# Optimization experiments

Hardware: AMD Instinct MI355X
Metric: run time of the kernel (lower is better)

## Reference

```python
import jax, jax.numpy as jnp
import numpy as np

N_NODES = 100_000
N_EDGES = 1_600_000
N_GRAPHS = 512
D_NODE = 128
H = 128
L_EXTRA = 2  # model_layer - 1


def _bn(x, g, b, eps=1e-5):
    # BatchNorm1d, training-mode math (biased batch variance), eval dropout = identity
    mu = jnp.mean(x, axis=0)
    var = jnp.var(x, axis=0)
    return g * (x - mu) * jax.lax.rsqrt(var + eps) + b


def _gin_conv(x, src, dst, W1, b1, bng, bnb, W2, b2):
    # GINConv (eps=0): mlp(x + sum_{j->i} x_j); mlp = Lin -> BN -> ReLU -> Lin
    agg = jax.ops.segment_sum(x[src], dst, num_segments=x.shape[0])
    h = x + agg
    h = jax.nn.relu(_bn(h @ W1 + b1, bng, bnb))
    return h @ W2 + b2


def setup_inputs():
    key = jax.random.key(0)
    ks = jax.random.split(key, 24)
    s = 0.05
    d = {}
    d["x"] = jax.random.normal(ks[0], (N_NODES, D_NODE), dtype=jnp.float32)
    d["edge_index"] = jax.random.randint(ks[1], (2, N_EDGES), 0, N_NODES, dtype=jnp.int32)
    d["batch"] = jnp.sort(jax.random.randint(ks[2], (N_NODES,), 0, N_GRAPHS, dtype=jnp.int32))
    d["vn_emb"] = jax.random.normal(ks[3], (1, H)) * s
    # conv1 MLP: Linear(D_NODE, 2H) -> BN -> ReLU -> Linear(2H, H)
    d["c1_W1"] = jax.random.normal(ks[4], (D_NODE, 2 * H)) * s
    d["c1_b1"] = jnp.zeros((2 * H,))
    d["c1_bng"] = jnp.ones((2 * H,))
    d["c1_bnb"] = jnp.zeros((2 * H,))
    d["c1_W2"] = jax.random.normal(ks[5], (2 * H, H)) * s
    d["c1_b2"] = jnp.zeros((H,))
    d["bn1_g"] = jnp.ones((H,))
    d["bn1_b"] = jnp.zeros((H,))
    # stacked extra GIN layers (model_layer - 1)
    d["cW1"] = jax.random.normal(ks[6], (L_EXTRA, H, 2 * H)) * s
    d["cb1"] = jnp.zeros((L_EXTRA, 2 * H))
    d["cbng"] = jnp.ones((L_EXTRA, 2 * H))
    d["cbnb"] = jnp.zeros((L_EXTRA, 2 * H))
    d["cW2"] = jax.random.normal(ks[7], (L_EXTRA, 2 * H, H)) * s
    d["cb2"] = jnp.zeros((L_EXTRA, H))
    d["bns_g"] = jnp.ones((L_EXTRA, H))
    d["bns_b"] = jnp.zeros((L_EXTRA, H))
    # virtual node MLP: Lin(H,2H)->BN->ReLU->Lin(2H,H)->BN->ReLU->Dropout
    d["vW1"] = jax.random.normal(ks[8], (H, 2 * H)) * s
    d["vb1"] = jnp.zeros((2 * H,))
    d["vbn1_g"] = jnp.ones((2 * H,))
    d["vbn1_b"] = jnp.zeros((2 * H,))
    d["vW2"] = jax.random.normal(ks[9], (2 * H, H)) * s
    d["vb2"] = jnp.zeros((H,))
    d["vbn2_g"] = jnp.ones((H,))
    d["vbn2_b"] = jnp.zeros((H,))
    return d


def reference(x, edge_index, batch, vn_emb, c1_W1, c1_b1, c1_bng, c1_bnb, c1_W2, c1_b2,
              bn1_g, bn1_b, cW1, cb1, cbng, cbnb, cW2, cb2, bns_g, bns_b,
              vW1, vb1, vbn1_g, vbn1_b, vW2, vb2, vbn2_g, vbn2_b):
    src, dst = edge_index[0], edge_index[1]
    # virtual node feature per graph: Embedding(1, H) indexed with zeros
    vfeat = jnp.broadcast_to(vn_emb[0], (N_GRAPHS, H))
    # layer 1: dropout is identity in eval mode
    post = jax.nn.relu(_bn(_gin_conv(x, src, dst, c1_W1, c1_b1, c1_bng, c1_bnb, c1_W2, c1_b2), bn1_g, bn1_b))
    for i in range(L_EXTRA):
        post = post + vfeat[batch]                       # virtual-node broadcast
        post = _bn(_gin_conv(post, src, dst, cW1[i], cb1[i], cbng[i], cbnb[i], cW2[i], cb2[i]), bns_g[i], bns_b[i])
        if i < L_EXTRA - 1:
            post = jax.nn.relu(post)
            pooled = jax.ops.segment_sum(post, batch, num_segments=N_GRAPHS)  # GlobalAddPool
            z = pooled + vfeat
            z = jax.nn.relu(_bn(z @ vW1 + vb1, vbn1_g, vbn1_b))
            vfeat = jax.nn.relu(_bn(z @ vW2 + vb2, vbn2_g, vbn2_b))
    # readout: global mean pool over nodes per graph
    counts = jax.ops.segment_sum(jnp.ones((x.shape[0],), post.dtype), batch, num_segments=N_GRAPHS)
    out = jax.ops.segment_sum(post, batch, num_segments=N_GRAPHS) / jnp.maximum(counts, 1.0)[:, None]
    return out
```

## Files before the change

### kernel.cpp

```cpp
#include <hip/hip_runtime.h>

#define NN 100000
#define NE 1600000
#define NG 512
#define DH 128
#define DH2 256
#define SCB 98
#define NSTRIPE 32

typedef __attribute__((ext_vector_type(8))) _Float16 h8;
typedef __attribute__((ext_vector_type(2))) _Float16 h2;
typedef __attribute__((ext_vector_type(4))) float f4;

static inline size_t align256(size_t x) { return (x + 255) & ~size_t(255); }

__global__ __launch_bounds__(256) void countslot_k(const int* __restrict__ ei,
                                                   int* __restrict__ cursor,
                                                   int* __restrict__ slot) {
    int i = blockIdx.x * blockDim.x + threadIdx.x;
    int stride = gridDim.x * blockDim.x;
    for (int e = i; e < NE; e += stride)
        slot[e] = atomicAdd(&cursor[ei[NE + e]], 1);
}

__global__ __launch_bounds__(256) void place_k(const int* __restrict__ ei,
                                               const int* __restrict__ rowptr,
                                               const int* __restrict__ slot,
                                               int* __restrict__ esrc) {
    int i = blockIdx.x * blockDim.x + threadIdx.x;
    int stride = gridDim.x * blockDim.x;
    for (int e = i; e < NE; e += stride)
        esrc[rowptr[ei[NE + e]] + slot[e]] = ei[e];
}

__global__ __launch_bounds__(256) void scan1_k(const int* __restrict__ deg,
                                               int* __restrict__ part) {
    int i0 = blockIdx.x * 1024 + threadIdx.x * 4;
    int s = 0;
    if (i0 < NN) {
        int4 v = *(const int4*)(deg + i0);
        s = v.x + v.y + v.z + v.w;
    }
#pragma unroll
    for (int o = 1; o < 64; o <<= 1) s += __shfl_xor(s, o);
    __shared__ int ws[4];
    if ((threadIdx.x & 63) == 0) ws[threadIdx.x >> 6] = s;
    __syncthreads();
    if (threadIdx.x == 0) part[blockIdx.x] = ws[0] + ws[1] + ws[2] + ws[3];
}

__global__ void scan2_k(int* __restrict__ part, int* __restrict__ rowptr,
                        const int* __restrict__ batch, int* __restrict__ gcnt) {
    int t = threadIdx.x;
    __shared__ int wtot[2];
    int v = 0, s = 0;
    if (t < 128) {
        v = (t < SCB) ? part[t] : 0;
        s = v;
#pragma unroll
        for (int o = 1; o < 64; o <<= 1) {
            int u = __shfl_up(s, o);
            if ((t & 63) >= o) s += u;
        }
        if ((t & 63) == 63) wtot[t >> 6] = s;
    }
    __syncthreads();
    if (t < 128) {
        if (t >= 64) s += wtot[0];
        if (t < SCB) part[t] = s - v;
        if (t == SCB - 1) rowptr[NN] = s;
    }
    for (int g = t; g < NG; g += 256) {
        int lo = 0, hi = NN;
        while (lo < hi) { int m = (lo + hi) >> 1; if (batch[m] < g) lo = m + 1; else hi = m; }
        int b0 = lo;
        lo = 0; hi = NN;
        int g1 = g + 1;
        while (lo < hi) { int m = (lo + hi) >> 1; if (batch[m] < g1) lo = m + 1; else hi = m; }
        gcnt[g] = lo - b0;
    }
}

__global__ __launch_bounds__(256) void scan3_k(const int* __restrict__ deg,
                                               const int* __restrict__ part,
                                               int* __restrict__ rowptr) {
    int t = threadIdx.x;
    int i0 = blockIdx.x * 1024 + t * 4;
    int4 v = {0, 0, 0, 0};
    if (i0 < NN) v = *(const int4*)(deg + i0);
    int s = v.x + v.y + v.z + v.w;
    __shared__ int sc[256];
    sc[t] = s;
    __syncthreads();
    for (int o = 1; o < 256; o <<= 1) {
        int add = (t >= o) ? sc[t - o] : 0;
        __syncthreads();
        sc[t] += add;
        __syncthreads();
    }
    int excl = (t ? sc[t - 1] : 0) + part[blockIdx.x];
    if (i0 < NN) {
        int4 r;
        r.x = excl;
        r.y = excl + v.x;
        r.z = excl + v.x + v.y;
        r.w = excl + v.x + v.y + v.z;
        *(int4*)(rowptr + i0) = r;
    }
}

__global__ void castx_k(const float* __restrict__ x, _Float16* __restrict__ xh,
                        const float* __restrict__ emb, _Float16* __restrict__ vfeat) {
    int i = blockIdx.x * blockDim.x + threadIdx.x;
    if (i < NG * 16) {
        const float* e = emb + (i & 15) * 8;
        h8 v = {(_Float16)e[0], (_Float16)e[1], (_Float16)e[2], (_Float16)e[3],
                (_Float16)e[4], (_Float16)e[5], (_Float16)e[6], (_Float16)e[7]};
        ((h8*)vfeat)[i] = v;
    }
    if (i >= NN * 16) return;
    const float4* s = (const float4*)x + i * 2;
    float4 p = s[0], q = s[1];
    h8 h = {(_Float16)p.x, (_Float16)p.y, (_Float16)p.z, (_Float16)p.w,
            (_Float16)q.x, (_Float16)q.y, (_Float16)q.z, (_Float16)q.w};
    ((h8*)xh)[i] = h;
}

__global__ void zin_k(const float* __restrict__ pooled, const _Float16* __restrict__ vf,
                      _Float16* __restrict__ zb) {
    int i = blockIdx.x * blockDim.x + threadIdx.x;
    if (i < NG * DH) zb[i] = (_Float16)(pooled[i] + (float)vf[i]);
}

__global__ void addvn_k(_Float16* __restrict__ x, const _Float16* __restrict__ vfeat,
                        const int* __restrict__ batch) {
    int i = blockIdx.x * blockDim.x + threadIdx.x;
    if (i >= NN * 16) return;
    int row = i >> 4;
    int bg = batch[row];
    h8 u = ((h8*)x)[i];
    h8 v = ((const h8*)vfeat)[bg * 16 + (i & 15)];
    h8 o;
#pragma unroll
    for (int e = 0; e < 8; e++) o[e] = (_Float16)((float)u[e] + (float)v[e]);
    ((h8*)x)[i] = o;
}

__global__ void finalout_k(const float* __restrict__ pooled2, const int* __restrict__ gcnt,
                           float* __restrict__ outp) {
    int i = blockIdx.x * blockDim.x + threadIdx.x;
    if (i >= NG * DH) return;
    float cnt = (float)gcnt[i >> 7];
    outp[i] = pooled2[i] / fmaxf(cnt, 1.0f);
}

struct WPack {
    const float* w[8];
    _Float16* wt[8];
    int K[8];
    int N[8];
};
__global__ void wtrans_k(WPack p) {
    int id = blockIdx.z;
    const float* W = p.w[id];
    _Float16* Wt = p.wt[id];
    int K = p.K[id], N = p.N[id];
    int n0 = blockIdx.x * 32, k0 = blockIdx.y * 32;
    if (n0 >= N || k0 >= K) return;
    __shared__ float t[32][33];
    int tx = threadIdx.x & 31, ty = threadIdx.x >> 5;
    for (int i = 0; i < 32; i += 8)
        t[ty + i][tx] = W[(size_t)(k0 + ty + i) * N + n0 + tx];
    __syncthreads();
    for (int i = 0; i < 32; i += 8)
        Wt[(size_t)(n0 + ty + i) * K + k0 + tx] = (_Float16)t[tx][ty + i];
}

__global__ __launch_bounds__(256) void agg_k(const _Float16* __restrict__ xin,
                                             const int* __restrict__ rowptr,
                                             const int* __restrict__ esrc,
                                             _Float16* __restrict__ out) {
    int wave = threadIdx.x >> 6, lane = threadIdx.x & 63;
    int node = blockIdx.x * 4 + wave;
    if (node >= NN) return;
    const h2* xr = (const h2*)xin;
    h2 self = xr[(size_t)node * 64 + lane];
    float a0 = (float)self.x, a1 = (float)self.y;
    int beg = rowptr[node], end = rowptr[node + 1];
    int j = beg;
    for (; j + 7 < end; j += 8) {
        int s0 = esrc[j],     s1 = esrc[j + 1], s2 = esrc[j + 2], s3 = esrc[j + 3];
        int s4 = esrc[j + 4], s5 = esrc[j + 5], s6 = esrc[j + 6], s7 = esrc[j + 7];
        h2 u0 = xr[(size_t)s0 * 64 + lane];
        h2 u1 = xr[(size_t)s1 * 64 + lane];
        h2 u2 = xr[(size_t)s2 * 64 + lane];
        h2 u3 = xr[(size_t)s3 * 64 + lane];
        h2 u4 = xr[(size_t)s4 * 64 + lane];
        h2 u5 = xr[(size_t)s5 * 64 + lane];
        h2 u6 = xr[(size_t)s6 * 64 + lane];
        h2 u7 = xr[(size_t)s7 * 64 + lane];
        a0 += ((float)u0.x + (float)u1.x) + ((float)u2.x + (float)u3.x)
            + ((float)u4.x + (float)u5.x) + ((float)u6.x + (float)u7.x);
        a1 += ((float)u0.y + (float)u1.y) + ((float)u2.y + (float)u3.y)
            + ((float)u4.y + (float)u5.y) + ((float)u6.y + (float)u7.y);
    }
    for (; j < end; j++) {
        h2 u = xr[(size_t)esrc[j] * 64 + lane];
        a0 += (float)u.x; a1 += (float)u.y;
    }
    h2 o; o.x = (_Float16)a0; o.y = (_Float16)a1;
    ((h2*)out)[(size_t)node * 64 + lane] = o;
}

__global__ __launch_bounds__(256, 3) void gemmA_k(
        const _Float16* __restrict__ A, const _Float16* __restrict__ Wt,
        const float* __restrict__ bias, _Float16* __restrict__ C,
        float* __restrict__ csum, float* __restrict__ csq, int M) {
    constexpr int K = 128, NCF = 256;
    constexpr int LDA = K + 8;
    __shared__ __align__(16) _Float16 As[64 * LDA];
    __shared__ __align__(16) _Float16 Ws[128 * LDA];
    const int tid = threadIdx.x;
    const int lane = tid & 63;
    const int wave = tid >> 6;
    const int wr = wave >> 1;
    const int wc = wave & 1;
    const int lm = lane & 15, lq = lane >> 4;
    const int mB = blockIdx.x * 64;

    const int sr = tid >> 4;
    const int sc = (tid & 15) * 8;
#pragma unroll
    for (int rr = 0; rr < 64; rr += 16) {
        int gr = mB + rr + sr; if (gr >= M) gr = M - 1;
        *(h8*)&As[(rr + sr) * LDA + sc] = *(const h8*)&A[(size_t)gr * K + sc];
    }
#pragma unroll
    for (int rr = 0; rr < 128; rr += 16)
        *(h8*)&Ws[(rr + sr) * LDA + sc] = *(const h8*)&Wt[(size_t)(rr + sr) * K + sc];
    __syncthreads();

    f4 acc[2][8];
#pragma unroll
    for (int i = 0; i < 2; i++)
#pragma unroll
        for (int jj = 0; jj < 8; jj++) acc[i][jj] = (f4){0.f, 0.f, 0.f, 0.f};
#pragma unroll
    for (int ct = 0; ct < 2; ct++) {
        if (ct) {
            __syncthreads();
#pragma unroll
            for (int rr = 0; rr < 128; rr += 16)
                *(h8*)&Ws[(rr + sr) * LDA + sc] =
                    *(const h8*)&Wt[(size_t)(128 + rr + sr) * K + sc];
            __syncthreads();
        }
#pragma unroll
        for (int ks = 0; ks < 4; ks++) {
            h8 af[2], bf[4];
#pragma unroll
            for (int i = 0; i < 2; i++)
                af[i] = *(const h8*)&As[(wr * 32 + i * 16 + lm) * LDA + ks * 32 + lq * 8];
#pragma unroll
            for (int j = 0; j < 4; j++)
                bf[j] = *(const h8*)&Ws[(wc * 64 + j * 16 + lm) * LDA + ks * 32 + lq * 8];
#pragma unroll
            for (int i = 0; i < 2; i++)
#pragma unroll
                for (int j = 0; j < 4; j++)
                    acc[i][ct * 4 + j] =
                        __builtin_amdgcn_mfma_f32_16x16x32_f16(af[i], bf[j], acc[i][ct * 4 + j], 0, 0, 0);
        }
    }

    float bv[8];
#pragma unroll
    for (int jj = 0; jj < 8; jj++) bv[jj] = bias[(jj >> 2) * 128 + wc * 64 + (jj & 3) * 16 + lm];
    float ls[8] = {0, 0, 0, 0, 0, 0, 0, 0}, lsq[8] = {0, 0, 0, 0, 0, 0, 0, 0};
    _Float16* Cs = As;
    const int trow = tid >> 4;
    const int tcol = (tid & 15) * 8;
#pragma unroll
    for (int half = 0; half < 2; half++) {
        __syncthreads();
#pragma unroll
        for (int i = 0; i < 2; i++) {
            int row = wr * 32 + i * 16 + lq * 4;
#pragma unroll
            for (int j = 0; j < 4; j++) {
                int jj = half * 4 + j;
#pragma unroll
                for (int r = 0; r < 4; r++) {
                    float v = acc[i][jj][r] + bv[jj];
                    Cs[(row + r) * LDA + wc * 64 + j * 16 + lm] = (_Float16)v;
                    if (mB + row + r < M) { ls[jj] += v; lsq[jj] += v * v; }
                }
            }
        }
        __syncthreads();
#pragma unroll
        for (int p = 0; p < 4; p++) {
            int row = p * 16 + trow;
            int grow = mB + row;
            if (grow < M) {
                h8 v = *(const h8*)&Cs[row * LDA + tcol];
                *(h8*)&C[(size_t)grow * NCF + half * 128 + tcol] = v;
            }
        }
    }
    const int stripe = blockIdx.x & (NSTRIPE - 1);
#pragma unroll
    for (int jj = 0; jj < 8; jj++) {
        float s = ls[jj], q = lsq[jj];
        s += __shfl_xor(s, 16); s += __shfl_xor(s, 32);
        q += __shfl_xor(q, 16); q += __shfl_xor(q, 32);
        if (lq == 0) {
            int col = (jj >> 2) * 128 + wc * 64 + (jj & 3) * 16 + lm;
            atomicAdd(&csum[stripe * NCF + col], s);
            atomicAdd(&csq[stripe * NCF + col], q);
        }
    }
}

__global__ __launch_bounds__(256, 3) void gemmB_k(
        const _Float16* __restrict__ A, const _Float16* __restrict__ Wt,
        const float* __restrict__ bias, _Float16* __restrict__ C,
        float* __restrict__ csum, float* __restrict__ csq, int M,
        const float* __restrict__ csumIn, const float* __restrict__ csqIn,
        const float* __restrict__ g, const float* __restrict__ b) {
    constexpr int K = 256, NCF = 128, BK = 128;
    constexpr int LDA = BK + 8;
    constexpr int LDW = BK + 4;
    __shared__ __align__(16) _Float16 As[64 * LDA];
    __shared__ __align__(16) _Float16 Ws[128 * LDW];
    __shared__ float s_sc[256], s_sh[256];
    const int tid = threadIdx.x;
    const int lane = tid & 63;
    const int wave = tid >> 6;
    const int wr = wave >> 1;
    const int wc = wave & 1;
    const int lm = lane & 15, lq = lane >> 4;
    const int mB = blockIdx.x * 64;
    const int n0 = wc * 64;

    {
        float s = 0.f, q = 0.f;
        for (int st = 0; st < NSTRIPE; st++) {
            s += csumIn[st * 256 + tid];
            q += csqIn[st * 256 + tid];
        }
        float invM = 1.0f / (float)M;
        float mean = s * invM;
        float var = q * invM - mean * mean;
        float scv = g[tid] * rsqrtf(var + 1e-5f);
        s_sc[tid] = scv;
        s_sh[tid] = b[tid] - mean * scv;
    }
    __syncthreads();

    f4 acc[2][4];
#pragma unroll
    for (int i = 0; i < 2; i++)
#pragma unroll
        for (int j = 0; j < 4; j++) acc[i][j] = (f4){0.f, 0.f, 0.f, 0.f};

    const int sr = tid >> 4;
    const int sc = (tid & 15) * 8;

    for (int kc = 0; kc < K; kc += BK) {
        if (kc) __syncthreads();
        float bscv[8], bshv[8];
#pragma unroll
        for (int e = 0; e < 8; e++) {
            bscv[e] = s_sc[kc + sc + e];
            bshv[e] = s_sh[kc + sc + e];
        }
#pragma unroll
        for (int rr = 0; rr < 64; rr += 16) {
            int gr = mB + rr + sr; if (gr >= M) gr = M - 1;
            h8 h = *(const h8*)&A[(size_t)gr * K + kc + sc];
#pragma unroll
            for (int e = 0; e < 8; e++)
                h[e] = (_Float16)fmaxf((float)h[e] * bscv[e] + bshv[e], 0.f);
            *(h8*)&As[(rr + sr) * LDA + sc] = h;
        }
#pragma unroll
        for (int rr = 0; rr < 128; rr += 16)
            *(h8*)&Ws[(rr + sr) * LDW + sc] =
                *(const h8*)&Wt[(size_t)(rr + sr) * K + kc + sc];
        __syncthreads();
#pragma unroll
        for (int ks = 0; ks < BK / 32; ks++) {
            h8 af[2], bf[4];
#pragma unroll
            for (int i = 0; i < 2; i++)
                af[i] = *(const h8*)&As[(wr * 32 + i * 16 + lm) * LDA + ks * 32 + lq * 8];
#pragma unroll
            for (int j = 0; j < 4; j++)
                bf[j] = *(const h8*)&Ws[(n0 + j * 16 + lm) * LDW + ks * 32 + lq * 8];
#pragma unroll
            for (int i = 0; i < 2; i++)
#pragma unroll
                for (int j = 0; j < 4; j++)
                    acc[i][j] = __builtin_amdgcn_mfma_f32_16x16x32_f16(af[i], bf[j], acc[i][j], 0, 0, 0);
        }
    }

    float bv[4];
#pragma unroll
    for (int j = 0; j < 4; j++) bv[j] = bias[n0 + j * 16 + lm];
    float ls[4] = {0, 0, 0, 0}, lsq[4] = {0, 0, 0, 0};
    __syncthreads();
    _Float16* Cs = As;
#pragma unroll
    for (int i = 0; i < 2; i++) {
        int row = wr * 32 + i * 16 + lq * 4;
        bool rv[4];
#pragma unroll
        for (int r = 0; r < 4; r++) rv[r] = (mB + row + r) < M;
#pragma unroll
        for (int j = 0; j < 4; j++) {
#pragma unroll
            for (int r = 0; r < 4; r++) {
                float v = acc[i][j][r] + bv[j];
                Cs[(row + r) * LDA + wc * 64 + j * 16 + lm] = (_Float16)v;
                if (rv[r]) { ls[j] += v; lsq[j] += v * v; }
            }
        }
    }
    const int stripe = blockIdx.x & (NSTRIPE - 1);
#pragma unroll
    for (int j = 0; j < 4; j++) {
        float s = ls[j], q = lsq[j];
        s += __shfl_xor(s, 16); s += __shfl_xor(s, 32);
        q += __shfl_xor(q, 16); q += __shfl_xor(q, 32);
        if (lq == 0) {
            atomicAdd(&csum[stripe * NCF + n0 + j * 16 + lm], s);
            atomicAdd(&csq[stripe * NCF + n0 + j * 16 + lm], q);
        }
    }
    __syncthreads();
    const int trow = tid >> 4;
    const int tcol = (tid & 15) * 8;
#pragma unroll
    for (int p = 0; p < 4; p++) {
        int row = p * 16 + trow;
        int grow = mB + row;
        if (grow < M) {
            h8 v = *(const h8*)&Cs[row * LDA + tcol];
            *(h8*)&C[(size_t)grow * NCF + tcol] = v;
        }
    }
}

__global__ void bnrelu_k(const _Float16* __restrict__ in, _Float16* __restrict__ out,
                         const float* __restrict__ csum, const float* __restrict__ csq,
                         const float* __restrict__ g, const float* __restrict__ b,
                         const _Float16* __restrict__ vfeat, const int* __restrict__ batch,
                         int M) {
    constexpr int PER = 16;
    __shared__ float s_sc[128], s_sh[128];
    if (threadIdx.x < 128) {
        int col = threadIdx.x;
        float s = 0.f, q = 0.f;
        for (int st = 0; st < NSTRIPE; st++) {
            s += csum[st * 128 + col];
            q += csq[st * 128 + col];
        }
        float invM = 1.0f / (float)M;
        float mean = s * invM;
        float var = q * invM - mean * mean;
        float scv = g[col] * rsqrtf(var + 1e-5f);
        s_sc[col] = scv;
        s_sh[col] = b[col] - mean * scv;
    }
    __syncthreads();
    int tid = blockIdx.x * blockDim.x + threadIdx.x;
    int c8 = tid % PER;
    int c0 = c8 * 8;
    float sc[8], sh[8];
#pragma unroll
    for (int e = 0; e < 8; e++) { sc[e] = s_sc[c0 + e]; sh[e] = s_sh[c0 + e]; }
    int total = M * PER;
    int stride = gridDim.x * blockDim.x;
    for (int i = tid; i < total; i += stride) {
        int row = i / PER;
        h8 u = ((const h8*)in)[i];
        h8 w;
        bool vn = (vfeat != nullptr);
        if (vn) w = ((const h8*)vfeat)[batch[row] * PER + c8];
        h8 o;
#pragma unroll
        for (int e = 0; e < 8; e++) {
            float vv = fmaxf((float)u[e] * sc[e] + sh[e], 0.f);
            if (vn) vv += (float)w[e];
            o[e] = (_Float16)vv;
        }
        ((h8*)out)[i] = o;
    }
}

__global__ __launch_bounds__(256) void bnpool_k(
        const _Float16* __restrict__ in, _Float16* __restrict__ out,
        const float* __restrict__ csum, const float* __restrict__ csq,
        const float* __restrict__ g, const float* __restrict__ b,
        const int* __restrict__ batch, float* __restrict__ pooled,
        int M, int relu) {
    __shared__ float s_sc[128], s_sh[128];
    if (threadIdx.x < 128) {
        int col = threadIdx.x;
        float s = 0.f, q = 0.f;
        for (int st = 0; st < NSTRIPE; st++) {
            s += csum[st * 128 + col];
            q += csq[st * 128 + col];
        }
        float invM = 1.0f / (float)M;
        float mean = s * invM;
        float var = q * invM - mean * mean;
        float scv = g[col] * rsqrtf(var + 1e-5f);
        s_sc[col] = scv;
        s_sh[col] = b[col] - mean * scv;
    }
    __syncthreads();
    int t = threadIdx.x;
    int c0 = (t & 63) * 2;
    int r0 = blockIdx.x * 128 + (t >> 6) * 32;
    float sc0 = s_sc[c0], h0 = s_sh[c0];
    float sc1 = s_sc[c0 + 1], h1 = s_sh[c0 + 1];
    int rend = r0 + 32; if (rend > M) rend = M;
    float a0 = 0.f, a1 = 0.f; int cur = -1;
    int r = r0;
    for (; r + 1 < rend; r += 2) {
        h2 ua = ((const h2*)in)[(size_t)r * 64 + (c0 >> 1)];
        h2 ub = ((const h2*)in)[(size_t)(r + 1) * 64 + (c0 >> 1)];
        int bga = batch[r], bgb = batch[r + 1];
        float va0 = (float)ua.x * sc0 + h0, va1 = (float)ua.y * sc1 + h1;
        float vb0 = (float)ub.x * sc0 + h0, vb1 = (float)ub.y * sc1 + h1;
        if (relu) {
            va0 = fmaxf(va0, 0.f); va1 = fmaxf(va1, 0.f);
            vb0 = fmaxf(vb0, 0.f); vb1 = fmaxf(vb1, 0.f);
        }
        if (out) {
            h2 oa; oa.x = (_Float16)va0; oa.y = (_Float16)va1;
            h2 ob; ob.x = (_Float16)vb0; ob.y = (_Float16)vb1;
            ((h2*)out)[(size_t)r * 64 + (c0 >> 1)] = oa;
            ((h2*)out)[(size_t)(r + 1) * 64 + (c0 >> 1)] = ob;
        }
        if (bga != cur) {
            if (cur >= 0) {
                atomicAdd(&pooled[(size_t)cur * DH + c0], a0);
                atomicAdd(&pooled[(size_t)cur * DH + c0 + 1], a1);
            }
            cur = bga; a0 = 0.f; a1 = 0.f;
        }
        a0 += va0; a1 += va1;
        if (bgb != cur) {
            atomicAdd(&pooled[(size_t)cur * DH + c0], a0);
            atomicAdd(&pooled[(size_t)cur * DH + c0 + 1], a1);
            cur = bgb; a0 = 0.f; a1 = 0.f;
        }
        a0 += vb0; a1 += vb1;
    }
    for (; r < rend; r++) {
        h2 u = ((const h2*)in)[(size_t)r * 64 + (c0 >> 1)];
        float v0 = (float)u.x * sc0 + h0;
        float v1 = (float)u.y * sc1 + h1;
        if (relu) { v0 = fmaxf(v0, 0.f); v1 = fmaxf(v1, 0.f); }
        if (out) { h2 o; o.x = (_Float16)v0; o.y = (_Float16)v1; ((h2*)out)[(size_t)r * 64 + (c0 >> 1)] = o; }
        int bg = batch[r];
        if (bg != cur) {
            if (cur >= 0) {
                atomicAdd(&pooled[(size_t)cur * DH + c0], a0);
                atomicAdd(&pooled[(size_t)cur * DH + c0 + 1], a1);
            }
            cur = bg; a0 = 0.f; a1 = 0.f;
        }
        a0 += v0; a1 += v1;
    }
    if (cur >= 0) {
        atomicAdd(&pooled[(size_t)cur * DH + c0], a0);
        atomicAdd(&pooled[(size_t)cur * DH + c0 + 1], a1);
    }
}

extern "C" void kernel_launch(void* const* d_in, const int* in_sizes, int n_in,
                              void* d_out, int out_size, void* d_ws, size_t ws_size,
                              hipStream_t stream) {
    const float* x      = (const float*)d_in[0];
    const int*   ei     = (const int*)d_in[1];
    const int*   batch  = (const int*)d_in[2];
    const float* vn_emb = (const float*)d_in[3];
    const float* c1_W1  = (const float*)d_in[4];
    const float* c1_b1  = (const float*)d_in[5];
    const float* c1_bng = (const float*)d_in[6];
    const float* c1_bnb = (const float*)d_in[7];
    const float* c1_W2  = (const float*)d_in[8];
    const float* c1_b2  = (const float*)d_in[9];
    const float* bn1_g  = (const float*)d_in[10];
    const float* bn1_b  = (const float*)d_in[11];
    const float* cW1    = (const float*)d_in[12];
    const float* cb1    = (const float*)d_in[13];
    const float* cbng   = (const float*)d_in[14];
    const float* cbnb   = (const float*)d_in[15];
    const float* cW2    = (const float*)d_in[16];
    const float* cb2    = (const float*)d_in[17];
    const float* bns_g  = (const float*)d_in[18];
    const float* bns_b  = (const float*)d_in[19];
    const float* vW1    = (const float*)d_in[20];
    const float* vb1    = (const float*)d_in[21];
    const float* vbn1_g = (const float*)d_in[22];
    const float* vbn1_b = (const float*)d_in[23];
    const float* vW2    = (const float*)d_in[24];
    const float* vb2    = (const float*)d_in[25];
    const float* vbn2_g = (const float*)d_in[26];
    const float* vbn2_b = (const float*)d_in[27];
    float* outp = (float*)d_out;
    (void)in_sizes; (void)n_in; (void)out_size; (void)ws_size;

    char* w = (char*)d_ws;
    size_t off = 0;
    auto carve = [&](size_t bytes) -> void* {
        void* p = w + off; off = align256(off + bytes); return p;
    };
    int*   cursor  = (int*)carve((size_t)NN * 4);
    float* pooled  = (float*)carve((size_t)NG * DH * 4);
    float* pooled2 = (float*)carve((size_t)NG * DH * 4);
    float *sA[3], *qA[3], *sB[3], *qB[3], *sV1, *qV1, *sV2, *qV2;
    for (int i = 0; i < 3; i++) {
        sA[i] = (float*)carve((size_t)NSTRIPE * 256 * 4);
        qA[i] = (float*)carve((size_t)NSTRIPE * 256 * 4);
    }
    for (int i = 0; i < 3; i++) {
        sB[i] = (float*)carve((size_t)NSTRIPE * 128 * 4);
        qB[i] = (float*)carve((size_t)NSTRIPE * 128 * 4);
    }
    sV1 = (float*)carve((size_t)NSTRIPE * 256 * 4);
    qV1 = (float*)carve((size_t)NSTRIPE * 256 * 4);
    sV2 = (float*)carve((size_t)NSTRIPE * 128 * 4);
    qV2 = (float*)carve((size_t)NSTRIPE * 128 * 4);
    size_t zbytes = off;
    int*   gcnt    = (int*)carve((size_t)NG * 4);
    int*   rowptr  = (int*)carve((size_t)(NN + 1) * 4);
    int*   slot    = (int*)carve((size_t)NE * 4);
    int*   esrc    = (int*)carve((size_t)NE * 4);
    int*   part    = (int*)carve((size_t)SCB * 4);
    _Float16* vfeat = (_Float16*)carve((size_t)NG * DH * 2);
    _Float16* zin   = (_Float16*)carve((size_t)NG * DH * 2);
    _Float16* zb    = (_Float16*)carve((size_t)NG * DH2 * 2);
    _Float16* vraw  = (_Float16*)carve((size_t)NG * DH * 2);
    _Float16* xh    = (_Float16*)carve((size_t)NN * DH * 2);
    _Float16* hb    = (_Float16*)carve((size_t)NN * DH * 2);
    _Float16* b1    = (_Float16*)carve((size_t)NN * DH2 * 2);
    _Float16* abuf  = (_Float16*)carve((size_t)NN * DH * 2);
    _Float16* Wt[8];
    for (int i = 0; i < 8; i++) Wt[i] = (_Float16*)carve((size_t)DH * DH2 * 2);

    WPack wp;
    wp.w[0] = c1_W1;            wp.K[0] = 128; wp.N[0] = 256;
    wp.w[1] = c1_W2;            wp.K[1] = 256; wp.N[1] = 128;
    wp.w[2] = cW1;              wp.K[2] = 128; wp.N[2] = 256;
    wp.w[3] = cW2;              wp.K[3] = 256; wp.N[3] = 128;
    wp.w[4] = cW1 + 128 * 256;  wp.K[4] = 128; wp.N[4] = 256;
    wp.w[5] = cW2 + 256 * 128;  wp.K[5] = 256; wp.N[5] = 128;
    wp.w[6] = vW1;              wp.K[6] = 128; wp.N[6] = 256;
    wp.w[7] = vW2;              wp.K[7] = 256; wp.N[7] = 128;
    for (int i = 0; i < 8; i++) wp.wt[i] = Wt[i];

    const int GB64 = (NN + 63) / 64;
    const int GB   = (NN + 127) / 128;
    const int GV64 = (NG + 63) / 64;

    hipMemsetAsync(d_ws, 0, zbytes, stream);
    countslot_k<<<782, 256, 0, stream>>>(ei, cursor, slot);
    scan1_k<<<SCB, 256, 0, stream>>>(cursor, part);
    scan2_k<<<1, 256, 0, stream>>>(part, rowptr, batch, gcnt);
    scan3_k<<<SCB, 256, 0, stream>>>(cursor, part, rowptr);
    place_k<<<782, 256, 0, stream>>>(ei, rowptr, slot, esrc);
    wtrans_k<<<dim3(8, 8, 8), 256, 0, stream>>>(wp);
    castx_k<<<(NN * 16 + 255) / 256, 256, 0, stream>>>(x, xh, vn_emb, vfeat);

    agg_k<<<NN / 4, 256, 0, stream>>>(xh, rowptr, esrc, hb);
    gemmA_k<<<GB64, 256, 0, stream>>>(hb, Wt[0], c1_b1, b1, sA[0], qA[0], NN);
    gemmB_k<<<GB64, 256, 0, stream>>>(b1, Wt[1], c1_b2, abuf, sB[0], qB[0], NN,
                                      sA[0], qA[0], c1_bng, c1_bnb);
    bnrelu_k<<<2048, 256, 0, stream>>>(abuf, abuf, sB[0], qB[0], bn1_g, bn1_b,
                                       vfeat, batch, NN);

    agg_k<<<NN / 4, 256, 0, stream>>>(abuf, rowptr, esrc, hb);
    gemmA_k<<<GB64, 256, 0, stream>>>(hb, Wt[2], cb1, b1, sA[1], qA[1], NN);
    gemmB_k<<<GB64, 256, 0, stream>>>(b1, Wt[3], cb2, abuf, sB[1], qB[1], NN,
                                      sA[1], qA[1], cbng, cbnb);
    bnpool_k<<<GB, 256, 0, stream>>>(abuf, abuf, sB[1], qB[1], bns_g, bns_b,
                                     batch, pooled, NN, 1);

    zin_k<<<(NG * DH + 255) / 256, 256, 0, stream>>>(pooled, vfeat, zin);
    gemmA_k<<<GV64, 256, 0, stream>>>(zin, Wt[6], vb1, zb, sV1, qV1, NG);
    gemmB_k<<<GV64, 256, 0, stream>>>(zb, Wt[7], vb2, vraw, sV2, qV2, NG,
                                      sV1, qV1, vbn1_g, vbn1_b);
    bnrelu_k<<<32, 256, 0, stream>>>(vraw, vfeat, sV2, qV2, vbn2_g, vbn2_b,
                                     nullptr, nullptr, NG);

    addvn_k<<<(NN * 16 + 255) / 256, 256, 0, stream>>>(abuf, vfeat, batch);
    agg_k<<<NN / 4, 256, 0, stream>>>(abuf, rowptr, esrc, hb);
    gemmA_k<<<GB64, 256, 0, stream>>>(hb, Wt[4], cb1 + 256, b1, sA[2], qA[2], NN);
    gemmB_k<<<GB64, 256, 0, stream>>>(b1, Wt[5], cb2 + 128, abuf, sB[2], qB[2], NN,
                                      sA[2], qA[2], cbng + 256, cbnb + 256);
    bnpool_k<<<GB, 256, 0, stream>>>(abuf, nullptr, sB[2], qB[2],
                                     bns_g + 128, bns_b + 128, batch, pooled2, NN, 0);

    finalout_k<<<(NG * DH + 255) / 256, 256, 0, stream>>>(pooled2, gcnt, outp);
}
```

Before: 703.8 us.

## Recompute first GEMM instead of storing the 256-wide intermediate to global memory

The first MLP GEMM now runs twice. A stats-only pass accumulates the BatchNorm sums without writing the intermediate. A fused kernel then recomputes it, applies BN and ReLU in shared memory, and runs the second GEMM straight from there. This removes the write and re-read of the NN×256 fp16 intermediate buffer. The cost is doubled first-GEMM compute, more shared memory, and lower occupancy (launch bounds drop from 3 to 2 blocks per CU).

```diff
diff --git a/kernel.cpp b/kernel.cpp
--- a/kernel.cpp
+++ b/kernel.cpp
@@ -212,11 +212,11 @@
     ((h2*)out)[(size_t)node * 64 + lane] = o;
 }
 
-__global__ __launch_bounds__(256, 3) void gemmA_k(
+__global__ __launch_bounds__(256, 3) void gemmS_k(
         const _Float16* __restrict__ A, const _Float16* __restrict__ Wt,
-        const float* __restrict__ bias, _Float16* __restrict__ C,
+        const float* __restrict__ bias,
         float* __restrict__ csum, float* __restrict__ csq, int M) {
-    constexpr int K = 128, NCF = 256;
+    constexpr int K = 128;
     constexpr int LDA = K + 8;
     __shared__ __align__(16) _Float16 As[64 * LDA];
     __shared__ __align__(16) _Float16 Ws[128 * LDA];
@@ -277,34 +277,17 @@
 #pragma unroll
     for (int jj = 0; jj < 8; jj++) bv[jj] = bias[(jj >> 2) * 128 + wc * 64 + (jj & 3) * 16 + lm];
     float ls[8] = {0, 0, 0, 0, 0, 0, 0, 0}, lsq[8] = {0, 0, 0, 0, 0, 0, 0, 0};
-    _Float16* Cs = As;
-    const int trow = tid >> 4;
-    const int tcol = (tid & 15) * 8;
-#pragma unroll
-    for (int half = 0; half < 2; half++) {
-        __syncthreads();
-#pragma unroll
-        for (int i = 0; i < 2; i++) {
-            int row = wr * 32 + i * 16 + lq * 4;
-#pragma unroll
-            for (int j = 0; j < 4; j++) {
-                int jj = half * 4 + j;
-#pragma unroll
-                for (int r = 0; r < 4; r++) {
+#pragma unroll
+    for (int i = 0; i < 2; i++) {
+        int row = wr * 32 + i * 16 + lq * 4;
+#pragma unroll
+        for (int jj = 0; jj < 8; jj++) {
+#pragma unroll
+            for (int r = 0; r < 4; r++) {
+                if (mB + row + r < M) {
                     float v = acc[i][jj][r] + bv[jj];
-                    Cs[(row + r) * LDA + wc * 64 + j * 16 + lm] = (_Float16)v;
-                    if (mB + row + r < M) { ls[jj] += v; lsq[jj] += v * v; }
+                    ls[jj] += v; lsq[jj] += v * v;
                 }
-            }
-        }
-        __syncthreads();
-#pragma unroll
-        for (int p = 0; p < 4; p++) {
-            int row = p * 16 + trow;
-            int grow = mB + row;
-            if (grow < M) {
-                h8 v = *(const h8*)&Cs[row * LDA + tcol];
-                *(h8*)&C[(size_t)grow * NCF + half * 128 + tcol] = v;
             }
         }
     }
@@ -316,23 +299,25 @@
         q += __shfl_xor(q, 16); q += __shfl_xor(q, 32);
         if (lq == 0) {
             int col = (jj >> 2) * 128 + wc * 64 + (jj & 3) * 16 + lm;
-            atomicAdd(&csum[stripe * NCF + col], s);
-            atomicAdd(&csq[stripe * NCF + col], q);
-        }
-    }
-}
-
-__global__ __launch_bounds__(256, 3) void gemmB_k(
-        const _Float16* __restrict__ A, const _Float16* __restrict__ Wt,
-        const float* __restrict__ bias, _Float16* __restrict__ C,
+            atomicAdd(&csum[stripe * 256 + col], s);
+            atomicAdd(&csq[stripe * 256 + col], q);
+        }
+    }
+}
+
+__global__ __launch_bounds__(256, 2) void gemmF_k(
+        const _Float16* __restrict__ A,
+        const _Float16* __restrict__ Wt1,
+        const _Float16* __restrict__ Wt2,
+        const float* __restrict__ b1v,
+        const float* __restrict__ b2v,
+        _Float16* __restrict__ C,
         float* __restrict__ csum, float* __restrict__ csq, int M,
         const float* __restrict__ csumIn, const float* __restrict__ csqIn,
         const float* __restrict__ g, const float* __restrict__ b) {
-    constexpr int K = 256, NCF = 128, BK = 128;
-    constexpr int LDA = BK + 8;
-    constexpr int LDW = BK + 4;
-    __shared__ __align__(16) _Float16 As[64 * LDA];
-    __shared__ __align__(16) _Float16 Ws[128 * LDW];
+    constexpr int LDA = 136, LDH = 264;
+    __shared__ __align__(16) _Float16 Hx[64 * LDH];
+    __shared__ __align__(16) _Float16 Ws[128 * LDA];
     __shared__ float s_sc[256], s_sh[256];
     const int tid = threadIdx.x;
     const int lane = tid & 63;
@@ -341,7 +326,6 @@
     const int wc = wave & 1;
     const int lm = lane & 15, lq = lane >> 4;
     const int mB = blockIdx.x * 64;
-    const int n0 = wc * 64;
 
     {
         float s = 0.f, q = 0.f;
@@ -356,62 +340,118 @@
         s_sc[tid] = scv;
         s_sh[tid] = b[tid] - mean * scv;
     }
-    __syncthreads();
-
-    f4 acc[2][4];
-#pragma unroll
-    for (int i = 0; i < 2; i++)
-#pragma unroll
-        for (int j = 0; j < 4; j++) acc[i][j] = (f4){0.f, 0.f, 0.f, 0.f};
 
     const int sr = tid >> 4;
     const int sc = (tid & 15) * 8;
-
-    for (int kc = 0; kc < K; kc += BK) {
-        if (kc) __syncthreads();
-        float bscv[8], bshv[8];
-#pragma unroll
-        for (int e = 0; e < 8; e++) {
-            bscv[e] = s_sc[kc + sc + e];
-            bshv[e] = s_sh[kc + sc + e];
-        }
-#pragma unroll
-        for (int rr = 0; rr < 64; rr += 16) {
-            int gr = mB + rr + sr; if (gr >= M) gr = M - 1;
-            h8 h = *(const h8*)&A[(size_t)gr * K + kc + sc];
-#pragma unroll
-            for (int e = 0; e < 8; e++)
-                h[e] = (_Float16)fmaxf((float)h[e] * bscv[e] + bshv[e], 0.f);
-            *(h8*)&As[(rr + sr) * LDA + sc] = h;
-        }
-#pragma unroll
-        for (int rr = 0; rr < 128; rr += 16)
-            *(h8*)&Ws[(rr + sr) * LDW + sc] =
-                *(const h8*)&Wt[(size_t)(rr + sr) * K + kc + sc];
-        __syncthreads();
-#pragma unroll
-        for (int ks = 0; ks < BK / 32; ks++) {
+#pragma unroll
+    for (int rr = 0; rr < 64; rr += 16) {
+        int gr = mB + rr + sr; if (gr >= M) gr = M - 1;
+        *(h8*)&Hx[(rr + sr) * LDA + sc] = *(const h8*)&A[(size_t)gr * 128 + sc];
+    }
+#pragma unroll
+    for (int rr = 0; rr < 128; rr += 16)
+        *(h8*)&Ws[(rr + sr) * LDA + sc] = *(const h8*)&Wt1[(size_t)(rr + sr) * 128 + sc];
+    __syncthreads();
+
+    f4 acc[2][8];
+#pragma unroll
+    for (int i = 0; i < 2; i++)
+#pragma unroll
+        for (int jj = 0; jj < 8; jj++) acc[i][jj] = (f4){0.f, 0.f, 0.f, 0.f};
+#pragma unroll
+    for (int ct = 0; ct < 2; ct++) {
+        if (ct) {
+            __syncthreads();
+#pragma unroll
+            for (int rr = 0; rr < 128; rr += 16)
+                *(h8*)&Ws[(rr + sr) * LDA + sc] =
+                    *(const h8*)&Wt1[(size_t)(128 + rr + sr) * 128 + sc];
+            __syncthreads();
+        }
+#pragma unroll
+        for (int ks = 0; ks < 4; ks++) {
             h8 af[2], bf[4];
 #pragma unroll
             for (int i = 0; i < 2; i++)
-                af[i] = *(const h8*)&As[(wr * 32 + i * 16 + lm) * LDA + ks * 32 + lq * 8];
+                af[i] = *(const h8*)&Hx[(wr * 32 + i * 16 + lm) * LDA + ks * 32 + lq * 8];
 #pragma unroll
             for (int j = 0; j < 4; j++)
-                bf[j] = *(const h8*)&Ws[(n0 + j * 16 + lm) * LDW + ks * 32 + lq * 8];
+                bf[j] = *(const h8*)&Ws[(wc * 64 + j * 16 + lm) * LDA + ks * 32 + lq * 8];
 #pragma unroll
             for (int i = 0; i < 2; i++)
 #pragma unroll
                 for (int j = 0; j < 4; j++)
-                    acc[i][j] = __builtin_amdgcn_mfma_f32_16x16x32_f16(af[i], bf[j], acc[i][j], 0, 0, 0);
-        }
-    }
-
-    float bv[4];
-#pragma unroll
-    for (int j = 0; j < 4; j++) bv[j] = bias[n0 + j * 16 + lm];
+                    acc[i][ct * 4 + j] =
+                        __builtin_amdgcn_mfma_f32_16x16x32_f16(af[i], bf[j], acc[i][ct * 4 + j], 0, 0, 0);
+        }
+    }
+    __syncthreads();
+
+    {
+        float bv1[8];
+#pragma unroll
+        for (int jj = 0; jj < 8; jj++)
+            bv1[jj] = b1v[(jj >> 2) * 128 + wc * 64 + (jj & 3) * 16 + lm];
+#pragma unroll
+        for (int i = 0; i < 2; i++) {
+            int row = wr * 32 + i * 16 + lq * 4;
+#pragma unroll
+            for (int jj = 0; jj < 8; jj++) {
+                int col = (jj >> 2) * 128 + wc * 64 + (jj & 3) * 16 + lm;
+                float scv = s_sc[col], shv = s_sh[col];
+#pragma unroll
+                for (int r = 0; r < 4; r++) {
+                    float v = acc[i][jj][r] + bv1[jj];
+                    v = fmaxf(v * scv + shv, 0.f);
+                    Hx[(row + r) * LDH + col] = (_Float16)v;
+                }
+            }
+        }
+    }
+#pragma unroll
+    for (int rr = 0; rr < 128; rr += 16)
+        *(h8*)&Ws[(rr + sr) * LDA + sc] = *(const h8*)&Wt2[(size_t)(rr + sr) * 256 + sc];
+    __syncthreads();
+
+    f4 acc2[2][4];
+#pragma unroll
+    for (int i = 0; i < 2; i++)
+#pragma unroll
+        for (int j = 0; j < 4; j++) acc2[i][j] = (f4){0.f, 0.f, 0.f, 0.f};
+#pragma unroll
+    for (int kc = 0; kc < 2; kc++) {
+        if (kc) {
+            __syncthreads();
+#pragma unroll
+            for (int rr = 0; rr < 128; rr += 16)
+                *(h8*)&Ws[(rr + sr) * LDA + sc] =
+                    *(const h8*)&Wt2[(size_t)(rr + sr) * 256 + 128 + sc];
+            __syncthreads();
+        }
+#pragma unroll
+        for (int ks = 0; ks < 4; ks++) {
+            h8 af[2], bf[4];
+#pragma unroll
+            for (int i = 0; i < 2; i++)
+                af[i] = *(const h8*)&Hx[(wr * 32 + i * 16 + lm) * LDH + kc * 128 + ks * 32 + lq * 8];
+#pragma unroll
+            for (int j = 0; j < 4; j++)
+                bf[j] = *(const h8*)&Ws[(wc * 64 + j * 16 + lm) * LDA + ks * 32 + lq * 8];
+#pragma unroll
+            for (int i = 0; i < 2; i++)
+#pragma unroll
+                for (int j = 0; j < 4; j++)
+                    acc2[i][j] = __builtin_amdgcn_mfma_f32_16x16x32_f16(af[i], bf[j], acc2[i][j], 0, 0, 0);
+        }
+    }
+
+    const int n0 = wc * 64;
+    float bv2[4];
+#pragma unroll
+    for (int j = 0; j < 4; j++) bv2[j] = b2v[n0 + j * 16 + lm];
     float ls[4] = {0, 0, 0, 0}, lsq[4] = {0, 0, 0, 0};
     __syncthreads();
-    _Float16* Cs = As;
+    _Float16* Cs = Hx;
 #pragma unroll
     for (int i = 0; i < 2; i++) {
         int row = wr * 32 + i * 16 + lq * 4;
@@ -422,7 +462,7 @@
         for (int j = 0; j < 4; j++) {
 #pragma unroll
             for (int r = 0; r < 4; r++) {
-                float v = acc[i][j][r] + bv[j];
+                float v = acc2[i][j][r] + bv2[j];
                 Cs[(row + r) * LDA + wc * 64 + j * 16 + lm] = (_Float16)v;
                 if (rv[r]) { ls[j] += v; lsq[j] += v * v; }
             }
@@ -435,8 +475,8 @@
         s += __shfl_xor(s, 16); s += __shfl_xor(s, 32);
         q += __shfl_xor(q, 16); q += __shfl_xor(q, 32);
         if (lq == 0) {
-            atomicAdd(&csum[stripe * NCF + n0 + j * 16 + lm], s);
-            atomicAdd(&csq[stripe * NCF + n0 + j * 16 + lm], q);
+            atomicAdd(&csum[stripe * 128 + n0 + j * 16 + lm], s);
+            atomicAdd(&csq[stripe * 128 + n0 + j * 16 + lm], q);
         }
     }
     __syncthreads();
@@ -448,7 +488,7 @@
         int grow = mB + row;
         if (grow < M) {
             h8 v = *(const h8*)&Cs[row * LDA + tcol];
-            *(h8*)&C[(size_t)grow * NCF + tcol] = v;
+            *(h8*)&C[(size_t)grow * 128 + tcol] = v;
         }
     }
 }
@@ -646,11 +686,9 @@
     int*   part    = (int*)carve((size_t)SCB * 4);
     _Float16* vfeat = (_Float16*)carve((size_t)NG * DH * 2);
     _Float16* zin   = (_Float16*)carve((size_t)NG * DH * 2);
-    _Float16* zb    = (_Float16*)carve((size_t)NG * DH2 * 2);
     _Float16* vraw  = (_Float16*)carve((size_t)NG * DH * 2);
     _Float16* xh    = (_Float16*)carve((size_t)NN * DH * 2);
     _Float16* hb    = (_Float16*)carve((size_t)NN * DH * 2);
-    _Float16* b1    = (_Float16*)carve((size_t)NN * DH2 * 2);
     _Float16* abuf  = (_Float16*)carve((size_t)NN * DH * 2);
     _Float16* Wt[8];
     for (int i = 0; i < 8; i++) Wt[i] = (_Float16*)carve((size_t)DH * DH2 * 2);
@@ -680,31 +718,31 @@
     castx_k<<<(NN * 16 + 255) / 256, 256, 0, stream>>>(x, xh, vn_emb, vfeat);
 
     agg_k<<<NN / 4, 256, 0, stream>>>(xh, rowptr, esrc, hb);
-    gemmA_k<<<GB64, 256, 0, stream>>>(hb, Wt[0], c1_b1, b1, sA[0], qA[0], NN);
-    gemmB_k<<<GB64, 256, 0, stream>>>(b1, Wt[1], c1_b2, abuf, sB[0], qB[0], NN,
-                                      sA[0], qA[0], c1_bng, c1_bnb);
+    gemmS_k<<<GB64, 256, 0, stream>>>(hb, Wt[0], c1_b1, sA[0], qA[0], NN);
+    gemmF_k<<<GB64, 256, 0, stream>>>(hb, Wt[0], Wt[1], c1_b1, c1_b2, abuf,
+                                      sB[0], qB[0], NN, sA[0], qA[0], c1_bng, c1_bnb);
     bnrelu_k<<<2048, 256, 0, stream>>>(abuf, abuf, sB[0], qB[0], bn1_g, bn1_b,
                                        vfeat, batch, NN);
 
     agg_k<<<NN / 4, 256, 0, stream>>>(abuf, rowptr, esrc, hb);
-    gemmA_k<<<GB64, 256, 0, stream>>>(hb, Wt[2], cb1, b1, sA[1], qA[1], NN);
-    gemmB_k<<<GB64, 256, 0, stream>>>(b1, Wt[3], cb2, abuf, sB[1], qB[1], NN,
-                                      sA[1], qA[1], cbng, cbnb);
+    gemmS_k<<<GB64, 256, 0, stream>>>(hb, Wt[2], cb1, sA[1], qA[1], NN);
+    gemmF_k<<<GB64, 256, 0, stream>>>(hb, Wt[2], Wt[3], cb1, cb2, abuf,
+                                      sB[1], qB[1], NN, sA[1], qA[1], cbng, cbnb);
     bnpool_k<<<GB, 256, 0, stream>>>(abuf, abuf, sB[1], qB[1], bns_g, bns_b,
                                      batch, pooled, NN, 1);
 
     zin_k<<<(NG * DH + 255) / 256, 256, 0, stream>>>(pooled, vfeat, zin);
-    gemmA_k<<<GV64, 256, 0, stream>>>(zin, Wt[6], vb1, zb, sV1, qV1, NG);
-    gemmB_k<<<GV64, 256, 0, stream>>>(zb, Wt[7], vb2, vraw, sV2, qV2, NG,
-                                      sV1, qV1, vbn1_g, vbn1_b);
+    gemmS_k<<<GV64, 256, 0, stream>>>(zin, Wt[6], vb1, sV1, qV1, NG);
+    gemmF_k<<<GV64, 256, 0, stream>>>(zin, Wt[6], Wt[7], vb1, vb2, vraw,
+                                      sV2, qV2, NG, sV1, qV1, vbn1_g, vbn1_b);
     bnrelu_k<<<32, 256, 0, stream>>>(vraw, vfeat, sV2, qV2, vbn2_g, vbn2_b,
                                      nullptr, nullptr, NG);
 
     addvn_k<<<(NN * 16 + 255) / 256, 256, 0, stream>>>(abuf, vfeat, batch);
     agg_k<<<NN / 4, 256, 0, stream>>>(abuf, rowptr, esrc, hb);
-    gemmA_k<<<GB64, 256, 0, stream>>>(hb, Wt[4], cb1 + 256, b1, sA[2], qA[2], NN);
-    gemmB_k<<<GB64, 256, 0, stream>>>(b1, Wt[5], cb2 + 128, abuf, sB[2], qB[2], NN,
-                                      sA[2], qA[2], cbng + 256, cbnb + 256);
+    gemmS_k<<<GB64, 256, 0, stream>>>(hb, Wt[4], cb1 + 256, sA[2], qA[2], NN);
+    gemmF_k<<<GB64, 256, 0, stream>>>(hb, Wt[4], Wt[5], cb1 + 256, cb2 + 128, abuf,
+                                      sB[2], qB[2], NN, sA[2], qA[2], cbng + 256, cbnb + 256);
     bnpool_k<<<GB, 256, 0, stream>>>(abuf, nullptr, sB[2], qB[2],
                                      bns_g + 128, bns_b + 128, batch, pooled2, NN, 0);
 
```

After: 708.6 us. About the same (+0.7%).

## Fuse CSR count, input cast and weight transpose; split atomic counters four ways

Applied to the files above, without the earlier changes.

The edge-counting kernel, the x/vfeat cast and the weight transpose are merged into one launch whose block ranges dispatch to the three jobs. The per-destination atomic counters are split into four copies indexed by edge position mod 4, which is meant to reduce atomic contention. The scan kernels now sum the four copies and emit per-copy row bases, which place_k uses. Edges are processed four per thread with int4 loads, at the cost of a larger cursor buffer and an extra rowbase array.

```diff
diff --git a/kernel.cpp b/kernel.cpp
--- a/kernel.cpp
+++ b/kernel.cpp
@@ -7,6 +7,9 @@
 #define DH2 256
 #define SCB 98
 #define NSTRIPE 32
+#define EB4 1563
+#define CB 6250
+#define WB 512
 
 typedef __attribute__((ext_vector_type(8))) _Float16 h8;
 typedef __attribute__((ext_vector_type(2))) _Float16 h2;
@@ -14,32 +17,94 @@
 
 static inline size_t align256(size_t x) { return (x + 255) & ~size_t(255); }
 
-__global__ __launch_bounds__(256) void countslot_k(const int* __restrict__ ei,
-                                                   int* __restrict__ cursor,
-                                                   int* __restrict__ slot) {
-    int i = blockIdx.x * blockDim.x + threadIdx.x;
-    int stride = gridDim.x * blockDim.x;
-    for (int e = i; e < NE; e += stride)
-        slot[e] = atomicAdd(&cursor[ei[NE + e]], 1);
+struct WPack {
+    const float* w[8];
+    _Float16* wt[8];
+    int K[8];
+    int N[8];
+};
+
+__global__ __launch_bounds__(256) void csrcast_k(
+        const int* __restrict__ ei, int* __restrict__ cursor, int* __restrict__ slot,
+        const float* __restrict__ x, _Float16* __restrict__ xh,
+        const float* __restrict__ emb, _Float16* __restrict__ vfeat,
+        WPack p) {
+    __shared__ float t[32][33];
+    int b = blockIdx.x;
+    if (b < EB4) {
+        int i = b * 256 + threadIdx.x;
+        int e = i * 4;
+        if (e >= NE) return;
+        int4 d = *(const int4*)(ei + NE + e);
+        int s0 = atomicAdd(&cursor[0 * NN + d.x], 1);
+        int s1 = atomicAdd(&cursor[1 * NN + d.y], 1);
+        int s2 = atomicAdd(&cursor[2 * NN + d.z], 1);
+        int s3 = atomicAdd(&cursor[3 * NN + d.w], 1);
+        int4 r; r.x = s0; r.y = s1; r.z = s2; r.w = s3;
+        *(int4*)(slot + e) = r;
+    } else if (b < EB4 + CB) {
+        int i = (b - EB4) * 256 + threadIdx.x;
+        if (i < NG * 16) {
+            const float* e = emb + (i & 15) * 8;
+            h8 v = {(_Float16)e[0], (_Float16)e[1], (_Float16)e[2], (_Float16)e[3],
+                    (_Float16)e[4], (_Float16)e[5], (_Float16)e[6], (_Float16)e[7]};
+            ((h8*)vfeat)[i] = v;
+        }
+        if (i >= NN * 16) return;
+        const float4* s = (const float4*)x + i * 2;
+        float4 pp = s[0], q = s[1];
+        h8 h = {(_Float16)pp.x, (_Float16)pp.y, (_Float16)pp.z, (_Float16)pp.w,
+                (_Float16)q.x, (_Float16)q.y, (_Float16)q.z, (_Float16)q.w};
+        ((h8*)xh)[i] = h;
+    } else {
+        int idx = b - (EB4 + CB);
+        int id = idx >> 6;
+        int rem = idx & 63;
+        const float* W = p.w[id];
+        _Float16* Wt = p.wt[id];
+        int K = p.K[id], N = p.N[id];
+        int n0 = (rem & 7) * 32, k0 = (rem >> 3) * 32;
+        if (n0 >= N || k0 >= K) return;
+        int tx = threadIdx.x & 31, ty = threadIdx.x >> 5;
+        for (int i = 0; i < 32; i += 8)
+            t[ty + i][tx] = W[(size_t)(k0 + ty + i) * N + n0 + tx];
+        __syncthreads();
+        for (int i = 0; i < 32; i += 8)
+            Wt[(size_t)(n0 + ty + i) * K + k0 + tx] = (_Float16)t[tx][ty + i];
+    }
 }
 
 __global__ __launch_bounds__(256) void place_k(const int* __restrict__ ei,
-                                               const int* __restrict__ rowptr,
+                                               const int* __restrict__ rowbase,
                                                const int* __restrict__ slot,
                                                int* __restrict__ esrc) {
     int i = blockIdx.x * blockDim.x + threadIdx.x;
-    int stride = gridDim.x * blockDim.x;
-    for (int e = i; e < NE; e += stride)
-        esrc[rowptr[ei[NE + e]] + slot[e]] = ei[e];
-}
-
-__global__ __launch_bounds__(256) void scan1_k(const int* __restrict__ deg,
+    int e = i * 4;
+    if (e >= NE) return;
+    int4 d = *(const int4*)(ei + NE + e);
+    int4 sl = *(const int4*)(slot + e);
+    int4 sr = *(const int4*)(ei + e);
+    int r0 = rowbase[0 * NN + d.x];
+    int r1 = rowbase[1 * NN + d.y];
+    int r2 = rowbase[2 * NN + d.z];
+    int r3 = rowbase[3 * NN + d.w];
+    esrc[r0 + sl.x] = sr.x;
+    esrc[r1 + sl.y] = sr.y;
+    esrc[r2 + sl.z] = sr.z;
+    esrc[r3 + sl.w] = sr.w;
+}
+
+__global__ __launch_bounds__(256) void scan1_k(const int* __restrict__ cur,
                                                int* __restrict__ part) {
     int i0 = blockIdx.x * 1024 + threadIdx.x * 4;
     int s = 0;
     if (i0 < NN) {
-        int4 v = *(const int4*)(deg + i0);
-        s = v.x + v.y + v.z + v.w;
+        int4 a = *(const int4*)(cur + i0);
+        int4 b = *(const int4*)(cur + NN + i0);
+        int4 c = *(const int4*)(cur + 2 * NN + i0);
+        int4 d = *(const int4*)(cur + 3 * NN + i0);
+        s = (a.x + a.y + a.z + a.w) + (b.x + b.y + b.z + b.w)
+          + (c.x + c.y + c.z + c.w) + (d.x + d.y + d.z + d.w);
     }
 #pragma unroll
     for (int o = 1; o < 64; o <<= 1) s += __shfl_xor(s, o);
@@ -81,14 +146,25 @@
     }
 }
 
-__global__ __launch_bounds__(256) void scan3_k(const int* __restrict__ deg,
+__global__ __launch_bounds__(256) void scan3_k(const int* __restrict__ cur,
                                                const int* __restrict__ part,
-                                               int* __restrict__ rowptr) {
+                                               int* __restrict__ rowptr,
+                                               int* __restrict__ rowbase) {
     int t = threadIdx.x;
     int i0 = blockIdx.x * 1024 + t * 4;
-    int4 v = {0, 0, 0, 0};
-    if (i0 < NN) v = *(const int4*)(deg + i0);
-    int s = v.x + v.y + v.z + v.w;
+    int4 c0 = {0,0,0,0}, c1 = {0,0,0,0}, c2 = {0,0,0,0}, c3 = {0,0,0,0};
+    if (i0 < NN) {
+        c0 = *(const int4*)(cur + i0);
+        c1 = *(const int4*)(cur + NN + i0);
+        c2 = *(const int4*)(cur + 2 * NN + i0);
+        c3 = *(const int4*)(cur + 3 * NN + i0);
+    }
+    int4 tot;
+    tot.x = c0.x + c1.x + c2.x + c3.x;
+    tot.y = c0.y + c1.y + c2.y + c3.y;
+    tot.z = c0.z + c1.z + c2.z + c3.z;
+    tot.w = c0.w + c1.w + c2.w + c3.w;
+    int s = tot.x + tot.y + tot.z + tot.w;
     __shared__ int sc[256];
     sc[t] = s;
     __syncthreads();
@@ -102,28 +178,18 @@
     if (i0 < NN) {
         int4 r;
         r.x = excl;
-        r.y = excl + v.x;
-        r.z = excl + v.x + v.y;
-        r.w = excl + v.x + v.y + v.z;
+        r.y = excl + tot.x;
+        r.z = r.y + tot.y;
+        r.w = r.z + tot.z;
         *(int4*)(rowptr + i0) = r;
-    }
-}
-
-__global__ void castx_k(const float* __restrict__ x, _Float16* __restrict__ xh,
-                        const float* __restrict__ emb, _Float16* __restrict__ vfeat) {
-    int i = blockIdx.x * blockDim.x + threadIdx.x;
-    if (i < NG * 16) {
-        const float* e = emb + (i & 15) * 8;
-        h8 v = {(_Float16)e[0], (_Float16)e[1], (_Float16)e[2], (_Float16)e[3],
-                (_Float16)e[4], (_Float16)e[5], (_Float16)e[6], (_Float16)e[7]};
-        ((h8*)vfeat)[i] = v;
-    }
-    if (i >= NN * 16) return;
-    const float4* s = (const float4*)x + i * 2;
-    float4 p = s[0], q = s[1];
-    h8 h = {(_Float16)p.x, (_Float16)p.y, (_Float16)p.z, (_Float16)p.w,
-            (_Float16)q.x, (_Float16)q.y, (_Float16)q.z, (_Float16)q.w};
-    ((h8*)xh)[i] = h;
+        *(int4*)(rowbase + i0) = r;
+        int4 b1v; b1v.x = r.x + c0.x; b1v.y = r.y + c0.y; b1v.z = r.z + c0.z; b1v.w = r.w + c0.w;
+        *(int4*)(rowbase + NN + i0) = b1v;
+        int4 b2v; b2v.x = b1v.x + c1.x; b2v.y = b1v.y + c1.y; b2v.z = b1v.z + c1.z; b2v.w = b1v.w + c1.w;
+        *(int4*)(rowbase + 2 * NN + i0) = b2v;
+        int4 b3v; b3v.x = b2v.x + c2.x; b3v.y = b2v.y + c2.y; b3v.z = b2v.z + c2.z; b3v.w = b2v.w + c2.w;
+        *(int4*)(rowbase + 3 * NN + i0) = b3v;
+    }
 }
 
 __global__ void zin_k(const float* __restrict__ pooled, const _Float16* __restrict__ vf,
@@ -152,28 +218,6 @@
     if (i >= NG * DH) return;
     float cnt = (float)gcnt[i >> 7];
     outp[i] = pooled2[i] / fmaxf(cnt, 1.0f);
-}
-
-struct WPack {
-    const float* w[8];
-    _Float16* wt[8];
-    int K[8];
-    int N[8];
-};
-__global__ void wtrans_k(WPack p) {
-    int id = blockIdx.z;
-    const float* W = p.w[id];
-    _Float16* Wt = p.wt[id];
-    int K = p.K[id], N = p.N[id];
-    int n0 = blockIdx.x * 32, k0 = blockIdx.y * 32;
-    if (n0 >= N || k0 >= K) return;
-    __shared__ float t[32][33];
-    int tx = threadIdx.x & 31, ty = threadIdx.x >> 5;
-    for (int i = 0; i < 32; i += 8)
-        t[ty + i][tx] = W[(size_t)(k0 + ty + i) * N + n0 + tx];
-    __syncthreads();
-    for (int i = 0; i < 32; i += 8)
-        Wt[(size_t)(n0 + ty + i) * K + k0 + tx] = (_Float16)t[tx][ty + i];
 }
 
 __global__ __launch_bounds__(256) void agg_k(const _Float16* __restrict__ xin,
@@ -622,7 +666,7 @@
     auto carve = [&](size_t bytes) -> void* {
         void* p = w + off; off = align256(off + bytes); return p;
     };
-    int*   cursor  = (int*)carve((size_t)NN * 4);
+    int*   cursor  = (int*)carve((size_t)4 * NN * 4);
     float* pooled  = (float*)carve((size_t)NG * DH * 4);
     float* pooled2 = (float*)carve((size_t)NG * DH * 4);
     float *sA[3], *qA[3], *sB[3], *qB[3], *sV1, *qV1, *sV2, *qV2;
@@ -641,6 +685,7 @@
     size_t zbytes = off;
     int*   gcnt    = (int*)carve((size_t)NG * 4);
     int*   rowptr  = (int*)carve((size_t)(NN + 1) * 4);
+    int*   rowbase = (int*)carve((size_t)4 * NN * 4);
     int*   slot    = (int*)carve((size_t)NE * 4);
     int*   esrc    = (int*)carve((size_t)NE * 4);
     int*   part    = (int*)carve((size_t)SCB * 4);
@@ -671,13 +716,11 @@
     const int GV64 = (NG + 63) / 64;
 
     hipMemsetAsync(d_ws, 0, zbytes, stream);
-    countslot_k<<<782, 256, 0, stream>>>(ei, cursor, slot);
+    csrcast_k<<<EB4 + CB + WB, 256, 0, stream>>>(ei, cursor, slot, x, xh, vn_emb, vfeat, wp);
     scan1_k<<<SCB, 256, 0, stream>>>(cursor, part);
     scan2_k<<<1, 256, 0, stream>>>(part, rowptr, batch, gcnt);
-    scan3_k<<<SCB, 256, 0, stream>>>(cursor, part, rowptr);
-    place_k<<<782, 256, 0, stream>>>(ei, rowptr, slot, esrc);
-    wtrans_k<<<dim3(8, 8, 8), 256, 0, stream>>>(wp);
-    castx_k<<<(NN * 16 + 255) / 256, 256, 0, stream>>>(x, xh, vn_emb, vfeat);
+    scan3_k<<<SCB, 256, 0, stream>>>(cursor, part, rowptr, rowbase);
+    place_k<<<EB4, 256, 0, stream>>>(ei, rowbase, slot, esrc);
 
     agg_k<<<NN / 4, 256, 0, stream>>>(xh, rowptr, esrc, hb);
     gemmA_k<<<GB64, 256, 0, stream>>>(hb, Wt[0], c1_b1, b1, sA[0], qA[0], NN);
```

Result: faster. 685.1 us (-2.7%).
